# Optimization experiments

Measured on AMD Instinct MI355X. Metric: run time of the kernel, lower is better.

Reference implementation:

```python
import jax, jax.numpy as jnp
import numpy as np

NUM_GENES = 978
EMBED_DIM = 301
NUM_HEADS = 4
EMBED_DIM_HEADS = 48
N_NODES = 10000
N_EDGES = 320000


def setup_inputs() -> dict:
    key = jax.random.key(0)
    k1, k2, k3, k4 = jax.random.split(key, 4)
    x = jax.random.normal(k1, (N_NODES, NUM_GENES), dtype=jnp.float32)
    edge_index = jax.random.randint(k2, (2, N_EDGES), 0, N_NODES, dtype=jnp.int64)
    edge_weight = jax.random.uniform(k3, (N_EDGES,), dtype=jnp.float32)
    # GCNConv params: glorot-ish linear weight and zero bias
    W = jax.random.normal(k4, (NUM_GENES, EMBED_DIM), dtype=jnp.float32) * 0.03
    b = jnp.zeros((EMBED_DIM,), dtype=jnp.float32)
    return {"x": x, "edge_index": edge_index, "edge_weight": edge_weight, "W": W, "b": b}


def reference(x, edge_index, edge_weight, W, b):
    N = x.shape[0]
    src, dst = edge_index[0], edge_index[1]
    # GCNConv default: add self-loops with weight 1
    loop = jnp.arange(N, dtype=src.dtype)
    src_f = jnp.concatenate([src, loop])
    dst_f = jnp.concatenate([dst, loop])
    w_f = jnp.concatenate([edge_weight, jnp.ones((N,), dtype=edge_weight.dtype)])
    # symmetric normalization: deg over target nodes
    deg = jax.ops.segment_sum(w_f, dst_f, num_segments=N)
    deg_inv_sqrt = jnp.where(deg > 0, jax.lax.rsqrt(deg), 0.0)
    norm = deg_inv_sqrt[src_f] * w_f * deg_inv_sqrt[dst_f]  # [E+N]
    h = x @ W  # [N, EMBED_DIM]
    # gather source features, scale, scatter-add into targets
    out = jax.ops.segment_sum(norm[:, None] * h[src_f], dst_f, num_segments=N)
    out = out + b
    out = jax.nn.relu(out)
    # unsqueeze(1), unsqueeze(3), repeat(1, H, 1, dph) with H=4, dph=48//4=12
    rep = EMBED_DIM_HEADS // NUM_HEADS
    out = jnp.broadcast_to(out[:, None, :, None], (N, NUM_HEADS, EMBED_DIM, rep))
    return out
```

## Files before the change

kernel.cpp:

```cpp
#include <hip/hip_runtime.h>
#include <math.h>

#define NGENES 978
#define EDIM   301
#define NNODES 10000
#define NEDGES 320000
#define KPAD   992
#define NPAD   320
#define MPAD   10112

typedef float f4v __attribute__((ext_vector_type(4)));
typedef short s8v __attribute__((ext_vector_type(8)));

__device__ __forceinline__ void split_bf16(float v, short& hi, short& lo) {
    unsigned int b = __float_as_uint(v);
    hi = (short)(b >> 16);
    float hif = __uint_as_float(b & 0xFFFF0000u);
    float lof = v - hif;
    lo = (short)(__float_as_uint(lof) >> 16);
}

__global__ void prep_init(const unsigned int* __restrict__ ei, int* flag,
                          float* deg, int* cnt, int* cur) {
    int i = blockIdx.x * blockDim.x + threadIdx.x;
    if (i < NNODES) { deg[i] = 1.0f; cnt[i] = 0; cur[i] = 0; }
    if (blockIdx.x == 0 && threadIdx.x < 64) {
        unsigned int v = ei[2 * threadIdx.x + 1];
        unsigned long long nz = __ballot(v != 0u);
        if (threadIdx.x == 0) *flag = (nz == 0ULL) ? 1 : 0;
    }
}

__device__ __forceinline__ int load_idx(const void* ei, long long i, int is64) {
    return is64 ? (int)((const long long*)ei)[i] : ((const int*)ei)[i];
}

__global__ void accum_deg(const void* __restrict__ ei, const float* __restrict__ w,
                          float* deg, int* cnt, const int* __restrict__ flag) {
    int i = blockIdx.x * blockDim.x + threadIdx.x;
    if (i >= NEDGES) return;
    int is64 = *flag;
    int d = load_idx(ei, (long long)NEDGES + i, is64);
    atomicAdd(&deg[d], w[i]);
    atomicAdd(&cnt[d], 1);
}

__global__ __launch_bounds__(1024) void scan_dinv(const int* __restrict__ cnt,
                                                  int* __restrict__ base_,
                                                  const float* __restrict__ deg,
                                                  float* __restrict__ dinv) {
    __shared__ int part[1024];
    const int t = threadIdx.x;
    int local[10];
    int s = 0;
    #pragma unroll
    for (int j = 0; j < 10; ++j) {
        int idx = t * 10 + j;
        int v = (idx < NNODES) ? cnt[idx] : 0;
        local[j] = s;
        s += v;
    }
    part[t] = s;
    __syncthreads();
    for (int off = 1; off < 1024; off <<= 1) {
        int v = (t >= off) ? part[t - off] : 0;
        __syncthreads();
        part[t] += v;
        __syncthreads();
    }
    int carry = (t > 0) ? part[t - 1] : 0;
    #pragma unroll
    for (int j = 0; j < 10; ++j) {
        int idx = t * 10 + j;
        if (idx < NNODES) {
            base_[idx] = carry + local[j];
            float d = deg[idx];
            dinv[idx] = (d > 0.0f) ? rsqrtf(d) : 0.0f;
        }
    }
}

__global__ void fill_csr(const void* __restrict__ ei, const float* __restrict__ w,
                         const float* __restrict__ dinv, const int* __restrict__ base_,
                         int* cur, int* __restrict__ es, float* __restrict__ en,
                         const int* __restrict__ flag) {
    int e = blockIdx.x * blockDim.x + threadIdx.x;
    if (e >= NEDGES) return;
    int is64 = *flag;
    int s = load_idx(ei, e, is64);
    int d = load_idx(ei, (long long)NEDGES + e, is64);
    float nrm = dinv[s] * w[e] * dinv[d];
    int pos = base_[d] + atomicAdd(&cur[d], 1);
    es[pos] = s;
    en[pos] = nrm;
}

__global__ void cvt_x(const float* __restrict__ x, short* __restrict__ xh,
                      short* __restrict__ xl) {
    int idx = blockIdx.x * blockDim.x + threadIdx.x;
    if (idx >= NNODES * (KPAD / 8)) return;
    int r = idx / (KPAD / 8);
    int kc = (idx - r * (KPAD / 8)) * 8;
    s8v h8, l8;
    #pragma unroll
    for (int j = 0; j < 8; ++j) {
        int k = kc + j;
        float v = (k < NGENES) ? x[(size_t)r * NGENES + k] : 0.0f;
        short hi, lo;
        split_bf16(v, hi, lo);
        h8[j] = hi; l8[j] = lo;
    }
    *(s8v*)(xh + (size_t)r * KPAD + kc) = h8;
    *(s8v*)(xl + (size_t)r * KPAD + kc) = l8;
}

__global__ void cvt_w(const float* __restrict__ W, short* __restrict__ wh,
                      short* __restrict__ wl) {
    int idx = blockIdx.x * blockDim.x + threadIdx.x;
    if (idx >= NPAD * (KPAD / 8)) return;
    int n = idx / (KPAD / 8);
    int kc = (idx - n * (KPAD / 8)) * 8;
    s8v h8, l8;
    #pragma unroll
    for (int j = 0; j < 8; ++j) {
        int k = kc + j;
        float v = (n < EDIM && k < NGENES) ? W[(size_t)k * EDIM + n] : 0.0f;
        short hi, lo;
        split_bf16(v, hi, lo);
        h8[j] = hi; l8[j] = lo;
    }
    *(s8v*)(wh + (size_t)n * KPAD + kc) = h8;
    *(s8v*)(wl + (size_t)n * KPAD + kc) = l8;
}

__global__ __launch_bounds__(256) void gemm_bf16(const short* __restrict__ xh,
                                                 const short* __restrict__ xl,
                                                 const short* __restrict__ wh,
                                                 const short* __restrict__ wl,
                                                 float* __restrict__ h) {
    __shared__ short Ah[128 * 40], Al[128 * 40], Bh[64 * 40], Bl[64 * 40];
    const int tid  = threadIdx.x;
    const int lane = tid & 63;
    const int w    = tid >> 6;
    const int wm   = (w >> 1) * 64;
    const int wn   = (w & 1) * 32;
    const int bm   = blockIdx.y * 128;
    const int bn   = blockIdx.x * 64;
    const int l15  = lane & 15;
    const int g8   = (lane >> 4) * 8;

    f4v acc[4][2] = {};

    const int arow0 = tid >> 2;
    const int aslot = (tid & 3) * 8;

    for (int ks = 0; ks < KPAD / 32; ++ks) {
        const int k0 = ks * 32;
        #pragma unroll
        for (int q = 0; q < 2; ++q) {
            const int row = q * 64 + arow0;
            const size_t goff = (size_t)(bm + row) * KPAD + k0 + aslot;
            s8v vh = *(const s8v*)(xh + goff);
            s8v vl = *(const s8v*)(xl + goff);
            *(s8v*)&Ah[row * 40 + aslot] = vh;
            *(s8v*)&Al[row * 40 + aslot] = vl;
        }
        {
            const int row = tid >> 2;
            const size_t goff = (size_t)(bn + row) * KPAD + k0 + aslot;
            s8v vh = *(const s8v*)(wh + goff);
            s8v vl = *(const s8v*)(wl + goff);
            *(s8v*)&Bh[row * 40 + aslot] = vh;
            *(s8v*)&Bl[row * 40 + aslot] = vl;
        }
        __syncthreads();
        s8v ah[4], al[4], bh[2], bl[2];
        #pragma unroll
        for (int fn = 0; fn < 2; ++fn) {
            const int r = wn + fn * 16 + l15;
            bh[fn] = *(const s8v*)&Bh[r * 40 + g8];
            bl[fn] = *(const s8v*)&Bl[r * 40 + g8];
        }
        #pragma unroll
        for (int fm = 0; fm < 4; ++fm) {
            const int r = wm + fm * 16 + l15;
            ah[fm] = *(const s8v*)&Ah[r * 40 + g8];
            al[fm] = *(const s8v*)&Al[r * 40 + g8];
        }
        #pragma unroll
        for (int fm = 0; fm < 4; ++fm)
            #pragma unroll
            for (int fn = 0; fn < 2; ++fn) {
                acc[fm][fn] = __builtin_amdgcn_mfma_f32_16x16x32_bf16(ah[fm], bh[fn], acc[fm][fn], 0, 0, 0);
                acc[fm][fn] = __builtin_amdgcn_mfma_f32_16x16x32_bf16(ah[fm], bl[fn], acc[fm][fn], 0, 0, 0);
                acc[fm][fn] = __builtin_amdgcn_mfma_f32_16x16x32_bf16(al[fm], bh[fn], acc[fm][fn], 0, 0, 0);
            }
        __syncthreads();
    }
    const int mrb = (lane >> 4) * 4;
    #pragma unroll
    for (int fm = 0; fm < 4; ++fm)
        #pragma unroll
        for (int fn = 0; fn < 2; ++fn) {
            const int col = bn + wn + fn * 16 + l15;
            if (col >= EDIM) continue;
            #pragma unroll
            for (int r = 0; r < 4; ++r) {
                const int row = bm + wm + fm * 16 + mrb + r;
                if (row < NNODES) h[(size_t)row * EDIM + col] = acc[fm][fn][r];
            }
        }
}

__global__ __launch_bounds__(320) void gather_out(const float* __restrict__ h,
                                                  const float* __restrict__ dinv,
                                                  const float* __restrict__ bias,
                                                  const int* __restrict__ es,
                                                  const float* __restrict__ en,
                                                  const int* __restrict__ base_,
                                                  const int* __restrict__ cnt,
                                                  float4* __restrict__ out) {
    __shared__ int   s_src[64];
    __shared__ float s_nrm[64];
    __shared__ float row[EDIM];
    const int n = blockIdx.x;
    const int t = threadIdx.x;
    const int ce = (t < EDIM) ? t : 0;

    const float dn = dinv[n];
    float acc = h[(size_t)n * EDIM + ce] * (dn * dn) + bias[ce];

    const int cnt_n = cnt[n];
    const int b0 = base_[n];
    for (int e0 = 0; e0 < cnt_n; e0 += 64) {
        const int m = min(64, cnt_n - e0);
        if (t < m) { s_src[t] = es[b0 + e0 + t]; s_nrm[t] = en[b0 + e0 + t]; }
        __syncthreads();
        int e = 0;
        for (; e + 4 <= m; e += 4) {
            int   s0 = s_src[e],     s1 = s_src[e + 1], s2 = s_src[e + 2], s3 = s_src[e + 3];
            float w0 = s_nrm[e],     w1 = s_nrm[e + 1], w2 = s_nrm[e + 2], w3 = s_nrm[e + 3];
            float v0 = h[(size_t)s0 * EDIM + ce];
            float v1 = h[(size_t)s1 * EDIM + ce];
            float v2 = h[(size_t)s2 * EDIM + ce];
            float v3 = h[(size_t)s3 * EDIM + ce];
            acc = fmaf(w0, v0, acc); acc = fmaf(w1, v1, acc);
            acc = fmaf(w2, v2, acc); acc = fmaf(w3, v3, acc);
        }
        for (; e < m; ++e) acc = fmaf(s_nrm[e], h[(size_t)s_src[e] * EDIM + ce], acc);
        __syncthreads();
    }

    if (t < EDIM) row[t] = fmaxf(acc, 0.0f);
    __syncthreads();

    float4* o = out + (size_t)n * 4 * 903;
    for (int p = t; p < 903; p += 320) {
        const float v = row[p / 3];
        const float4 vv = make_float4(v, v, v, v);
        o[p] = vv; o[903 + p] = vv; o[1806 + p] = vv; o[2709 + p] = vv;
    }
}

extern "C" void kernel_launch(void* const* d_in, const int* in_sizes, int n_in,
                              void* d_out, int out_size, void* d_ws, size_t ws_size,
                              hipStream_t stream) {
    const float* x  = (const float*)d_in[0];
    const void*  ei = d_in[1];
    const float* ew = (const float*)d_in[2];
    const float* W  = (const float*)d_in[3];
    const float* b  = (const float*)d_in[4];

    char* p = (char*)d_ws;
    float* deg  = (float*)p;                 p += 40960;
    float* dinv = (float*)p;                 p += 40960;
    int*   cnt  = (int*)p;                   p += 40960;
    int*   base_= (int*)p;                   p += 40960;
    int*   cur  = (int*)p;                   p += 40960;
    int*   flag = (int*)p;                   p += 256;
    int*   es   = (int*)p;                   p += (size_t)NEDGES * 4;
    float* en   = (float*)p;                 p += (size_t)NEDGES * 4;
    float* h    = (float*)p;                 p += (size_t)NNODES * EDIM * 4;
    short* xh   = (short*)p;                 p += (size_t)MPAD * KPAD * 2;
    short* xl   = (short*)p;                 p += (size_t)MPAD * KPAD * 2;
    short* wh   = (short*)p;                 p += (size_t)NPAD * KPAD * 2;
    short* wl   = (short*)p;                 p += (size_t)NPAD * KPAD * 2;

    prep_init<<<40, 256, 0, stream>>>((const unsigned int*)ei, flag, deg, cnt, cur);
    accum_deg<<<(NEDGES + 255) / 256, 256, 0, stream>>>(ei, ew, deg, cnt, flag);
    scan_dinv<<<1, 1024, 0, stream>>>(cnt, base_, deg, dinv);
    fill_csr<<<(NEDGES + 255) / 256, 256, 0, stream>>>(ei, ew, dinv, base_, cur, es, en, flag);

    cvt_x<<<(NNODES * (KPAD / 8) + 255) / 256, 256, 0, stream>>>(x, xh, xl);
    cvt_w<<<(NPAD * (KPAD / 8) + 255) / 256, 256, 0, stream>>>(W, wh, wl);

    dim3 ggrid(NPAD / 64, MPAD / 128);
    gemm_bf16<<<ggrid, 256, 0, stream>>>(xh, xl, wh, wl, h);

    gather_out<<<NNODES, 320, 0, stream>>>(h, dinv, b, es, en, base_, cnt, (float4*)d_out);
    (void)in_sizes; (void)n_in; (void)out_size; (void)ws_size;
}
```

Baseline: 763.8 us.

## Pad h to 320 columns and gather with float4 rows split across edge groups

The GEMM now writes h with a padded row stride of 320, so padded columns hold zeros. The gather kernel splits its 320 threads into 4 edge groups of 80 threads. Each thread loads an aligned float4 of a source row, and the four partial sums are reduced through shared memory. Edge source index and norm are packed into one int2 array so each edge needs a single load, and the x and W conversion kernels are merged into one launch. The goal is to cut gather memory transactions and the shared-memory staging syncs, at the cost of a larger h buffer and a shared reduction step.

```diff
diff --git a/kernel.cpp b/kernel.cpp
--- a/kernel.cpp
+++ b/kernel.cpp
@@ -8,6 +8,7 @@
 #define KPAD   992
 #define NPAD   320
 #define MPAD   10112
+#define HP     320
 
 typedef float f4v __attribute__((ext_vector_type(4)));
 typedef short s8v __attribute__((ext_vector_type(8)));
@@ -82,7 +83,7 @@
 
 __global__ void fill_csr(const void* __restrict__ ei, const float* __restrict__ w,
                          const float* __restrict__ dinv, const int* __restrict__ base_,
-                         int* cur, int* __restrict__ es, float* __restrict__ en,
+                         int* cur, int2* __restrict__ ee,
                          const int* __restrict__ flag) {
     int e = blockIdx.x * blockDim.x + threadIdx.x;
     if (e >= NEDGES) return;
@@ -91,46 +92,45 @@
     int d = load_idx(ei, (long long)NEDGES + e, is64);
     float nrm = dinv[s] * w[e] * dinv[d];
     int pos = base_[d] + atomicAdd(&cur[d], 1);
-    es[pos] = s;
-    en[pos] = nrm;
-}
-
-__global__ void cvt_x(const float* __restrict__ x, short* __restrict__ xh,
-                      short* __restrict__ xl) {
+    ee[pos] = make_int2(s, __float_as_int(nrm));
+}
+
+#define XCH (NNODES * (KPAD / 8))
+#define WCH (NPAD * (KPAD / 8))
+__global__ void cvt_xw(const float* __restrict__ x, const float* __restrict__ W,
+                       short* __restrict__ xh, short* __restrict__ xl,
+                       short* __restrict__ wh, short* __restrict__ wl) {
     int idx = blockIdx.x * blockDim.x + threadIdx.x;
-    if (idx >= NNODES * (KPAD / 8)) return;
-    int r = idx / (KPAD / 8);
-    int kc = (idx - r * (KPAD / 8)) * 8;
-    s8v h8, l8;
-    #pragma unroll
-    for (int j = 0; j < 8; ++j) {
-        int k = kc + j;
-        float v = (k < NGENES) ? x[(size_t)r * NGENES + k] : 0.0f;
-        short hi, lo;
-        split_bf16(v, hi, lo);
-        h8[j] = hi; l8[j] = lo;
-    }
-    *(s8v*)(xh + (size_t)r * KPAD + kc) = h8;
-    *(s8v*)(xl + (size_t)r * KPAD + kc) = l8;
-}
-
-__global__ void cvt_w(const float* __restrict__ W, short* __restrict__ wh,
-                      short* __restrict__ wl) {
-    int idx = blockIdx.x * blockDim.x + threadIdx.x;
-    if (idx >= NPAD * (KPAD / 8)) return;
-    int n = idx / (KPAD / 8);
-    int kc = (idx - n * (KPAD / 8)) * 8;
-    s8v h8, l8;
-    #pragma unroll
-    for (int j = 0; j < 8; ++j) {
-        int k = kc + j;
-        float v = (n < EDIM && k < NGENES) ? W[(size_t)k * EDIM + n] : 0.0f;
-        short hi, lo;
-        split_bf16(v, hi, lo);
-        h8[j] = hi; l8[j] = lo;
-    }
-    *(s8v*)(wh + (size_t)n * KPAD + kc) = h8;
-    *(s8v*)(wl + (size_t)n * KPAD + kc) = l8;
+    if (idx < XCH) {
+        int r = idx / (KPAD / 8);
+        int kc = (idx - r * (KPAD / 8)) * 8;
+        s8v h8, l8;
+        #pragma unroll
+        for (int j = 0; j < 8; ++j) {
+            int k = kc + j;
+            float v = (k < NGENES) ? x[(size_t)r * NGENES + k] : 0.0f;
+            short hi, lo;
+            split_bf16(v, hi, lo);
+            h8[j] = hi; l8[j] = lo;
+        }
+        *(s8v*)(xh + (size_t)r * KPAD + kc) = h8;
+        *(s8v*)(xl + (size_t)r * KPAD + kc) = l8;
+    } else if (idx < XCH + WCH) {
+        int wi = idx - XCH;
+        int n = wi / (KPAD / 8);
+        int kc = (wi - n * (KPAD / 8)) * 8;
+        s8v h8, l8;
+        #pragma unroll
+        for (int j = 0; j < 8; ++j) {
+            int k = kc + j;
+            float v = (n < EDIM && k < NGENES) ? W[(size_t)k * EDIM + n] : 0.0f;
+            short hi, lo;
+            split_bf16(v, hi, lo);
+            h8[j] = hi; l8[j] = lo;
+        }
+        *(s8v*)(wh + (size_t)n * KPAD + kc) = h8;
+        *(s8v*)(wl + (size_t)n * KPAD + kc) = l8;
+    }
 }
 
 __global__ __launch_bounds__(256) void gemm_bf16(const short* __restrict__ xh,
@@ -203,11 +203,10 @@
         #pragma unroll
         for (int fn = 0; fn < 2; ++fn) {
             const int col = bn + wn + fn * 16 + l15;
-            if (col >= EDIM) continue;
             #pragma unroll
             for (int r = 0; r < 4; ++r) {
                 const int row = bm + wm + fm * 16 + mrb + r;
-                if (row < NNODES) h[(size_t)row * EDIM + col] = acc[fm][fn][r];
+                if (row < NNODES) h[(size_t)row * HP + col] = acc[fm][fn][r];
             }
         }
 }
@@ -215,50 +214,49 @@
 __global__ __launch_bounds__(320) void gather_out(const float* __restrict__ h,
                                                   const float* __restrict__ dinv,
                                                   const float* __restrict__ bias,
-                                                  const int* __restrict__ es,
-                                                  const float* __restrict__ en,
+                                                  const int2* __restrict__ ee,
                                                   const int* __restrict__ base_,
                                                   const int* __restrict__ cnt,
                                                   float4* __restrict__ out) {
-    __shared__ int   s_src[64];
-    __shared__ float s_nrm[64];
-    __shared__ float row[EDIM];
-    const int n = blockIdx.x;
-    const int t = threadIdx.x;
-    const int ce = (t < EDIM) ? t : 0;
-
-    const float dn = dinv[n];
-    float acc = h[(size_t)n * EDIM + ce] * (dn * dn) + bias[ce];
-
-    const int cnt_n = cnt[n];
+    __shared__ float red[4][HP];
+    __shared__ float row[HP];
+    const int n  = blockIdx.x;
+    const int t  = threadIdx.x;
+    const int g  = t / 80;
+    const int gt = t - g * 80;
+
     const int b0 = base_[n];
-    for (int e0 = 0; e0 < cnt_n; e0 += 64) {
-        const int m = min(64, cnt_n - e0);
-        if (t < m) { s_src[t] = es[b0 + e0 + t]; s_nrm[t] = en[b0 + e0 + t]; }
-        __syncthreads();
-        int e = 0;
-        for (; e + 4 <= m; e += 4) {
-            int   s0 = s_src[e],     s1 = s_src[e + 1], s2 = s_src[e + 2], s3 = s_src[e + 3];
-            float w0 = s_nrm[e],     w1 = s_nrm[e + 1], w2 = s_nrm[e + 2], w3 = s_nrm[e + 3];
-            float v0 = h[(size_t)s0 * EDIM + ce];
-            float v1 = h[(size_t)s1 * EDIM + ce];
-            float v2 = h[(size_t)s2 * EDIM + ce];
-            float v3 = h[(size_t)s3 * EDIM + ce];
-            acc = fmaf(w0, v0, acc); acc = fmaf(w1, v1, acc);
-            acc = fmaf(w2, v2, acc); acc = fmaf(w3, v3, acc);
-        }
-        for (; e < m; ++e) acc = fmaf(s_nrm[e], h[(size_t)s_src[e] * EDIM + ce], acc);
-        __syncthreads();
-    }
-
-    if (t < EDIM) row[t] = fmaxf(acc, 0.0f);
+    const int cn = cnt[n];
+    float4 acc = make_float4(0.f, 0.f, 0.f, 0.f);
+    for (int e = g; e < cn; e += 4) {
+        int2 p = ee[b0 + e];
+        float nr = __int_as_float(p.y);
+        float4 v = *(const float4*)(h + (size_t)p.x * HP + 4 * gt);
+        acc.x = fmaf(nr, v.x, acc.x);
+        acc.y = fmaf(nr, v.y, acc.y);
+        acc.z = fmaf(nr, v.z, acc.z);
+        acc.w = fmaf(nr, v.w, acc.w);
+    }
+    *(float4*)&red[g][4 * gt] = acc;
     __syncthreads();
+    if (t < HP) {
+        float dn = dinv[n];
+        float s = red[0][t] + red[1][t] + red[2][t] + red[3][t]
+                + h[(size_t)n * HP + t] * (dn * dn)
+                + ((t < EDIM) ? bias[t] : 0.0f);
+        row[t] = fmaxf(s, 0.0f);
+    }
+    __syncthreads();
 
     float4* o = out + (size_t)n * 4 * 903;
-    for (int p = t; p < 903; p += 320) {
-        const float v = row[p / 3];
-        const float4 vv = make_float4(v, v, v, v);
-        o[p] = vv; o[903 + p] = vv; o[1806 + p] = vv; o[2709 + p] = vv;
+    #pragma unroll
+    for (int q = 0; q < 3; ++q) {
+        int p = q * 320 + t;
+        if (p < 903) {
+            const float v = row[p / 3];
+            const float4 vv = make_float4(v, v, v, v);
+            o[p] = vv; o[903 + p] = vv; o[1806 + p] = vv; o[2709 + p] = vv;
+        }
     }
 }
 
@@ -278,9 +276,8 @@
     int*   base_= (int*)p;                   p += 40960;
     int*   cur  = (int*)p;                   p += 40960;
     int*   flag = (int*)p;                   p += 256;
-    int*   es   = (int*)p;                   p += (size_t)NEDGES * 4;
-    float* en   = (float*)p;                 p += (size_t)NEDGES * 4;
-    float* h    = (float*)p;                 p += (size_t)NNODES * EDIM * 4;
+    int2*  ee   = (int2*)p;                  p += (size_t)NEDGES * 8;
+    float* h    = (float*)p;                 p += (size_t)NNODES * HP * 4;
     short* xh   = (short*)p;                 p += (size_t)MPAD * KPAD * 2;
     short* xl   = (short*)p;                 p += (size_t)MPAD * KPAD * 2;
     short* wh   = (short*)p;                 p += (size_t)NPAD * KPAD * 2;
@@ -289,14 +286,13 @@
     prep_init<<<40, 256, 0, stream>>>((const unsigned int*)ei, flag, deg, cnt, cur);
     accum_deg<<<(NEDGES + 255) / 256, 256, 0, stream>>>(ei, ew, deg, cnt, flag);
     scan_dinv<<<1, 1024, 0, stream>>>(cnt, base_, deg, dinv);
-    fill_csr<<<(NEDGES + 255) / 256, 256, 0, stream>>>(ei, ew, dinv, base_, cur, es, en, flag);
-
-    cvt_x<<<(NNODES * (KPAD / 8) + 255) / 256, 256, 0, stream>>>(x, xh, xl);
-    cvt_w<<<(NPAD * (KPAD / 8) + 255) / 256, 256, 0, stream>>>(W, wh, wl);
+    fill_csr<<<(NEDGES + 255) / 256, 256, 0, stream>>>(ei, ew, dinv, base_, cur, ee, flag);
+
+    cvt_xw<<<(XCH + WCH + 255) / 256, 256, 0, stream>>>(x, W, xh, xl, wh, wl);
 
     dim3 ggrid(NPAD / 64, MPAD / 128);
     gemm_bf16<<<ggrid, 256, 0, stream>>>(xh, xl, wh, wl, h);
 
-    gather_out<<<NNODES, 320, 0, stream>>>(h, dinv, b, es, en, base_, cnt, (float4*)d_out);
+    gather_out<<<NNODES, 320, 0, stream>>>(h, dinv, b, ee, base_, cnt, (float4*)d_out);
     (void)in_sizes; (void)n_in; (void)out_size; (void)ws_size;
 }
```

Result: no change. 768.4 us (+0.6%).
